# Optimization experiments

Hardware: AMD Instinct MI355X
Metric: run time of the kernel (lower is better)

Reference implementation:

```python
import math
import jax, jax.numpy as jnp
import numpy as np

MAX_LEN = 1024

def _sinusoidal_pe(seq_len, d_model):
    pos = jnp.arange(seq_len, dtype=jnp.float32)[:, None]
    div = jnp.exp(jnp.arange(0, d_model, 2, dtype=jnp.float32) * (-math.log(10000.0) / d_model))
    ang = pos * div  # [S, D/2]
    pe = jnp.zeros((seq_len, d_model), dtype=jnp.float32)
    pe = pe.at[:, 0::2].set(jnp.sin(ang))
    pe = pe.at[:, 1::2].set(jnp.cos(ang))
    return pe

def setup_inputs() -> dict:
    key = jax.random.key(0)
    ks = jax.random.split(key, 4)
    B, S, D, H = 4, 1024, 1024, 16
    x = jax.random.normal(ks[0], (B, S, D), dtype=jnp.float32)
    gamma = jnp.ones((D,), dtype=jnp.float32)
    beta = jnp.zeros((D,), dtype=jnp.float32)
    w_pos = jax.random.normal(ks[1], (2 * D, D), dtype=jnp.float32) * (1.0 / math.sqrt(D))
    w_tok = jax.random.normal(ks[2], (3 * D, D), dtype=jnp.float32) * (1.0 / math.sqrt(D))
    bias_table = jax.random.normal(ks[3], (2 * MAX_LEN, H), dtype=jnp.float32) * 0.02
    return {"x": x, "gamma": gamma, "beta": beta, "w_pos": w_pos, "w_tok": w_tok, "bias_table": bias_table}

def reference(x, gamma, beta, w_pos, w_tok, bias_table):
    B, S, D = x.shape
    H = bias_table.shape[1]
    dh = D // H
    scale = 1.0 / math.sqrt(2 * dh)

    # untied positional scores (identical across batch)
    pe = _sinusoidal_pe(S, D)                      # [S, D]
    pos = pe @ w_pos.T                             # [S, 2D]
    pos_k, pos_q = pos[:, :D], pos[:, D:]
    pos_k = pos_k.reshape(S, H, dh)
    pos_q = pos_q.reshape(S, H, dh)
    pos_attn = jnp.einsum('qhd,khd->hqk', pos_q, pos_k)  # [H, S, S]

    # token scores
    mu = jnp.mean(x, axis=-1, keepdims=True)
    var = jnp.mean((x - mu) ** 2, axis=-1, keepdims=True)
    xn = (x - mu) / jnp.sqrt(var + 1e-5) * gamma + beta
    tok = xn @ w_tok.T                             # [B, S, 3D]
    tok_k, tok_q, tok_v = jnp.split(tok, 3, axis=-1)
    tok_k = tok_k.reshape(B, S, H, dh)
    tok_q = tok_q.reshape(B, S, H, dh)
    tok_v = tok_v.reshape(B, S, H, dh)
    tok_attn = jnp.einsum('bqhd,bkhd->bhqk', tok_q, tok_k)  # [B, H, S, S]

    attn = (tok_attn + pos_attn[None]) / scale

    # relative-position bias
    rel = jnp.arange(S)[None, :] - jnp.arange(S)[:, None] + MAX_LEN  # [S, S]
    bias = bias_table[rel]                         # [S, S, H]
    attn = attn + jnp.transpose(bias, (2, 0, 1))[None]

    attn = jax.nn.softmax(attn, axis=-1)
    out = jnp.einsum('bhqk,bkhd->bqhd', attn, tok_v)
    return out.reshape(B, S, D)
```

## Files before the change

### kernel.cpp

```cpp
#include <hip/hip_runtime.h>
#include <math.h>

#define SB 1024
#define DM 1024
#define BB 4
#define NH 16
#define DH 64
#define ML 1024

typedef __attribute__((ext_vector_type(8))) short short8;
typedef __attribute__((ext_vector_type(8))) _Float16 half8;
typedef __attribute__((ext_vector_type(4))) float f32x4;
typedef unsigned short u16;

__device__ __forceinline__ u16 f2bf(float x) {
  unsigned u = __float_as_uint(x);
  u += 0x7fffu + ((u >> 16) & 1u);
  return (u16)(u >> 16);
}
__device__ __forceinline__ float bf2f(u16 h) { return __uint_as_float((unsigned)h << 16); }

__device__ __forceinline__ void async16(void* lds, const void* g) {
  __builtin_amdgcn_global_load_lds(
      (const __attribute__((address_space(1))) unsigned*)g,
      (__attribute__((address_space(3))) unsigned*)lds, 16, 0, 0);
}


__device__ __forceinline__ void pack16_body(int rt, int t, const float* __restrict__ src,
    _Float16* __restrict__ dH, _Float16* __restrict__ dL, float scale) {
  int r16 = t >> 4, ks = t & 15;
  const float* sp = src + (size_t)(rt * 16 + r16) * 1024 + ks * 64;
  float v[64];
  #pragma unroll
  for (int i = 0; i < 16; ++i) {
    float4 f = *(const float4*)(sp + i * 4);
    v[i*4+0] = f.x; v[i*4+1] = f.y; v[i*4+2] = f.z; v[i*4+3] = f.w;
  }
  #pragma unroll
  for (int hf = 0; hf < 2; ++hf) {
    int kt = ks * 2 + hf;
    #pragma unroll
    for (int gg = 0; gg < 4; ++gg) {
      half8 hv, lv;
      #pragma unroll
      for (int j = 0; j < 8; ++j) {
        float x = v[hf * 32 + gg * 8 + j] * scale;
        _Float16 h = (_Float16)x;
        hv[j] = h;
        lv[j] = (_Float16)(x - (float)h);
      }
      size_t off = ((size_t)(rt * 32 + kt) * 64 + r16 + gg * 16) * 8;
      *(half8*)(dH + off) = hv;
      *(half8*)(dL + off) = lv;
    }
  }
}

__device__ __forceinline__ void pe_pack_body(int rt, int t,
    _Float16* __restrict__ dH, _Float16* __restrict__ dL) {
  int r16 = t >> 4, ks = t & 15;
  int p = rt * 16 + r16;
  float v[64];
  #pragma unroll
  for (int i = 0; i < 32; ++i) {
    int c0 = ks * 64 + 2 * i;
    float div = exp2f((float)c0 * (-0.01297628162065376f));
    float ang = (float)p * div;
    v[2*i]   = __sinf(ang);
    v[2*i+1] = __cosf(ang);
  }
  #pragma unroll
  for (int hf = 0; hf < 2; ++hf) {
    int kt = ks * 2 + hf;
    #pragma unroll
    for (int gg = 0; gg < 4; ++gg) {
      half8 hv, lv;
      #pragma unroll
      for (int j = 0; j < 8; ++j) {
        float x = v[hf * 32 + gg * 8 + j];
        _Float16 h = (_Float16)x;
        hv[j] = h;
        lv[j] = (_Float16)(x - (float)h);
      }
      size_t off = ((size_t)(rt * 32 + kt) * 64 + r16 + gg * 16) * 8;
      *(half8*)(dH + off) = hv;
      *(half8*)(dL + off) = lv;
    }
  }
}

__device__ __forceinline__ void ln_pack_body(int rt, int t, const float* __restrict__ x,
    const float* __restrict__ gamma, const float* __restrict__ beta,
    _Float16* __restrict__ dH, _Float16* __restrict__ dL) {
  int r16 = t >> 4, ks = t & 15;
  const float* sp = x + (size_t)(rt * 16 + r16) * 1024 + ks * 64;
  float v[64];
  float s1 = 0.f, s2 = 0.f;
  #pragma unroll
  for (int i = 0; i < 16; ++i) {
    float4 f = *(const float4*)(sp + i * 4);
    v[i*4+0] = f.x; v[i*4+1] = f.y; v[i*4+2] = f.z; v[i*4+3] = f.w;
    s1 += f.x + f.y + f.z + f.w;
    s2 += f.x*f.x + f.y*f.y + f.z*f.z + f.w*f.w;
  }
  #pragma unroll
  for (int off = 1; off < 16; off <<= 1) {
    s1 += __shfl_xor(s1, off, 64);
    s2 += __shfl_xor(s2, off, 64);
  }
  float mu = s1 * (1.0f / 1024.0f);
  float var = s2 * (1.0f / 1024.0f) - mu * mu;
  float rstd = rsqrtf(var + 1e-5f);
  #pragma unroll
  for (int hf = 0; hf < 2; ++hf) {
    int kt = ks * 2 + hf;
    #pragma unroll
    for (int gg = 0; gg < 4; ++gg) {
      const float* gp = gamma + ks * 64 + hf * 32 + gg * 8;
      const float* bp = beta  + ks * 64 + hf * 32 + gg * 8;
      half8 hv, lv;
      #pragma unroll
      for (int j = 0; j < 8; ++j) {
        float xn = (v[hf * 32 + gg * 8 + j] - mu) * rstd * gp[j] + bp[j];
        _Float16 h = (_Float16)xn;
        hv[j] = h;
        lv[j] = (_Float16)(xn - (float)h);
      }
      size_t off = ((size_t)(rt * 32 + kt) * 64 + r16 + gg * 16) * 8;
      *(half8*)(dH + off) = hv;
      *(half8*)(dL + off) = lv;
    }
  }
}

__global__ __launch_bounds__(256) void prep_all(
    const float* __restrict__ x, const float* __restrict__ gamma,
    const float* __restrict__ beta,
    const float* __restrict__ w_pos, const float* __restrict__ w_tok,
    _Float16* __restrict__ peH, _Float16* __restrict__ peL,
    _Float16* __restrict__ xnH, _Float16* __restrict__ xnL,
    _Float16* __restrict__ wpH, _Float16* __restrict__ wpL,
    _Float16* __restrict__ wtH, _Float16* __restrict__ wtL) {
  int bid = blockIdx.x;
  int t = threadIdx.x;
  if (bid < 64)       pe_pack_body(bid, t, peH, peL);
  else if (bid < 320) ln_pack_body(bid - 64, t, x, gamma, beta, xnH, xnL);
  else if (bid < 448) pack16_body(bid - 320, t, w_pos, wpH, wpL, 32.0f);
  else                pack16_body(bid - 448, t, w_tok, wtH, wtL, 32.0f);
}

__global__ __launch_bounds__(256, 2) void gemm16p(
    const _Float16* __restrict__ AtH, const _Float16* __restrict__ AtL,
    const _Float16* __restrict__ ApH, const _Float16* __restrict__ ApL,
    const _Float16* __restrict__ BtH, const _Float16* __restrict__ BtL,
    const _Float16* __restrict__ BpH, const _Float16* __restrict__ BpL,
    u16* __restrict__ KtfH, u16* __restrict__ KtfL,
    u16* __restrict__ KpfH, u16* __restrict__ KpfL,
    u16* __restrict__ QH, u16* __restrict__ QL,
    u16* __restrict__ pQH, u16* __restrict__ pQL,
    u16* __restrict__ vF, float sK, float sQ, float sV) {
  __shared__ _Float16 L[32 * 512];
  int t = threadIdx.x;
  int wv = t >> 6, lane = t & 63;
  int wm = wv >> 1, wn = wv & 1;
  int r16 = lane & 15, g = lane >> 4;

  int phys = blockIdx.x;
  int bid = (phys & 7) * 56 + (phys >> 3);
  bool isPos = (bid >= 384);
  int idx = isPos ? bid - 384 : bid;
  int n0, m0;
  const _Float16 *AH, *AL, *BH, *BL;
  if (isPos) { n0 = (idx & 7) * 256;  m0 = (idx >> 3) * 128;
               AH = ApH; AL = ApL; BH = BpH; BL = BpL; }
  else       { n0 = (idx % 12) * 256; m0 = (idx / 12) * 128;
               AH = AtH; AL = AtL; BH = BtH; BL = BtL; }
  int mt0 = m0 >> 4, nt0 = n0 >> 4;
  bool split = isPos || (n0 < 2048);

  f32x4 acc[4][8];
  #pragma unroll
  for (int i = 0; i < 4; ++i)
    #pragma unroll
    for (int j = 0; j < 8; ++j) acc[i][j] = (f32x4){0.f, 0.f, 0.f, 0.f};

  for (int kt = 0; kt < 32; ++kt) {
    __syncthreads();
    #pragma unroll
    for (int rd = 0; rd < 8; ++rd) {
      int ci = rd * 4 + wv;
      bool isAlo = (ci < 16) && (ci & 1);
      if (!split && isAlo) continue;
      const _Float16* src;
      if (ci < 16) {
        int mt = ci >> 1, pl = ci & 1;
        const _Float16* P = pl ? AL : AH;
        src = P + ((size_t)((mt0 + mt) * 32 + kt) * 64 + lane) * 8;
      } else {
        int nt = ci - 16;
        src = BH + ((size_t)((nt0 + nt) * 32 + kt) * 64 + lane) * 8;
      }
      async16(&L[ci * 512], src);
    }
    half8 blo[8];
    if (split) {
      #pragma unroll
      for (int j = 0; j < 8; ++j) {
        int ntg = nt0 + wn * 8 + j;
        blo[j] = *(const half8*)(BL + ((size_t)(ntg * 32 + kt) * 64 + lane) * 8);
      }
    }
    __syncthreads();

    half8 ah[4], al[4];
    #pragma unroll
    for (int i = 0; i < 4; ++i)
      ah[i] = *(const half8*)&L[(((wm * 4 + i) * 2 + 0) * 512) + lane * 8];
    if (split) {
      #pragma unroll
      for (int i = 0; i < 4; ++i)
        al[i] = *(const half8*)&L[(((wm * 4 + i) * 2 + 1) * 512) + lane * 8];
    }
    #pragma unroll
    for (int j = 0; j < 8; ++j) {
      half8 bh = *(const half8*)&L[((16 + wn * 8 + j) * 512) + lane * 8];
      #pragma unroll
      for (int i = 0; i < 4; ++i) {
        acc[i][j] = __builtin_amdgcn_mfma_f32_16x16x32_f16(ah[i], bh, acc[i][j], 0, 0, 0);
        if (split) {
          acc[i][j] = __builtin_amdgcn_mfma_f32_16x16x32_f16(al[i], bh, acc[i][j], 0, 0, 0);
          acc[i][j] = __builtin_amdgcn_mfma_f32_16x16x32_f16(ah[i], blo[j], acc[i][j], 0, 0, 0);
        }
      }
    }
  }

  int band = n0 >> 10;
  u16* fKH = isPos ? KpfH : KtfH;
  u16* fKL = isPos ? KpfL : KtfL;
  u16* qHo = isPos ? pQH  : QH;
  u16* qLo = isPos ? pQL  : QL;
  if (band == 1) {
    #pragma unroll
    for (int i = 0; i < 4; ++i)
      #pragma unroll
      for (int j = 0; j < 8; ++j) {
        int lc = (n0 & 1023) + wn * 128 + j * 16 + r16;
        #pragma unroll
        for (int reg = 0; reg < 4; ++reg) {
          int row = m0 + wm * 64 + i * 16 + g * 4 + reg;
          float cv = acc[i][j][reg] * sQ;
          u16 hi = f2bf(cv);
          qHo[(size_t)row * 1024 + lc] = hi;
          qLo[(size_t)row * 1024 + lc] = f2bf(cv - bf2f(hi));
        }
      }
  } else if (band == 0) {
    #pragma unroll
    for (int i = 0; i < 4; ++i)
      #pragma unroll
      for (int j = 0; j < 8; ++j) {
        int colg = n0 + wn * 128 + j * 16 + r16;
        int h = colg >> 6, dc = colg & 63;
        #pragma unroll
        for (int reg = 0; reg < 4; ++reg) {
          int row = m0 + wm * 64 + i * 16 + g * 4 + reg;
          int bhK = (row >> 10) * NH + h;
          size_t a = ((size_t)((bhK * 64 + ((row & 1023) >> 4)) * 2 + (dc >> 5)) << 9)
                   + ((row & 15) + 16 * ((dc >> 3) & 3)) * 8 + (dc & 7);
          float cv = acc[i][j][reg] * sK;
          u16 hi = f2bf(cv);
          fKH[a] = hi;
          fKL[a] = f2bf(cv - bf2f(hi));
        }
      }
  } else {
    #pragma unroll
    for (int i = 0; i < 4; ++i)
      #pragma unroll
      for (int j = 0; j < 8; ++j) {
        int colg = (n0 & 1023) + wn * 128 + j * 16 + r16;
        int h = colg >> 6, dc = colg & 63;
        #pragma unroll
        for (int reg = 0; reg < 4; ++reg) {
          int row = m0 + wm * 64 + i * 16 + g * 4 + reg;
          int s = row & 1023;
          size_t a = ((size_t)((((row >> 10) * NH + h) * 32 + (s >> 5)) * 4 + (dc >> 4)) << 9)
                   + ((s >> 3) & 3) * 128 + (s & 7) + (dc & 15) * 8;
          vF[a] = f2bf(acc[i][j][reg] * sV);
        }
      }
  }
}

__global__ __launch_bounds__(256, 2) void gemm16m(
    const _Float16* __restrict__ AtH, const _Float16* __restrict__ AtL,
    const _Float16* __restrict__ ApH, const _Float16* __restrict__ ApL,
    const float* __restrict__ Wt, const float* __restrict__ Wp,
    u16* __restrict__ KtfH, u16* __restrict__ KtfL,
    u16* __restrict__ KpfH, u16* __restrict__ KpfL,
    u16* __restrict__ QH, u16* __restrict__ QL,
    u16* __restrict__ pQH, u16* __restrict__ pQL,
    u16* __restrict__ vF, float sK, float sQ, float sV) {
  __shared__ _Float16 L[48 * 512];
  int t = threadIdx.x;
  int wv = t >> 6, lane = t & 63;
  int wm = wv >> 1, wn = wv & 1;
  int r16 = lane & 15, g = lane >> 4;

  int phys = blockIdx.x;
  int bid = (phys & 7) * 56 + (phys >> 3);
  bool isPos = (bid >= 384);
  int idx = isPos ? bid - 384 : bid;
  int n0, m0;
  const _Float16 *AH, *AL;
  const float* W;
  if (isPos) { n0 = (idx & 7) * 256;  m0 = (idx >> 3) * 128; AH = ApH; AL = ApL; W = Wp; }
  else       { n0 = (idx % 12) * 256; m0 = (idx / 12) * 128; AH = AtH; AL = AtL; W = Wt; }
  int mt0 = m0 >> 4, nt0 = n0 >> 4;
  bool split = isPos || (n0 < 2048);

  f32x4 acc[4][8];
  #pragma unroll
  for (int i = 0; i < 4; ++i)
    #pragma unroll
    for (int j = 0; j < 8; ++j) acc[i][j] = (f32x4){0.f, 0.f, 0.f, 0.f};

  for (int kt = 0; kt < 32; ++kt) {
    __syncthreads();
    #pragma unroll
    for (int rd = 0; rd < 4; ++rd) {
      int ci = rd * 4 + wv;
      int mt = ci >> 1, pl = ci & 1;
      if (!split && pl) continue;
      const _Float16* src = (pl ? AL : AH)
          + ((size_t)((mt0 + mt) * 32 + kt) * 64 + lane) * 8;
      async16(&L[ci * 512], src);
    }
    #pragma unroll
    for (int tt = 0; tt < 4; ++tt) {
      int nt = wv * 4 + tt;
      const float* wsrc = W + (size_t)((nt0 + nt) * 16 + r16) * 1024 + kt * 32 + g * 8;
      float4 w0 = *(const float4*)wsrc;
      float4 w1 = *(const float4*)(wsrc + 4);
      float wvv[8] = {w0.x, w0.y, w0.z, w0.w, w1.x, w1.y, w1.z, w1.w};
      half8 hv, lv;
      #pragma unroll
      for (int j = 0; j < 8; ++j) {
        float xx = wvv[j] * 32.0f;
        _Float16 h = (_Float16)xx;
        hv[j] = h;
        lv[j] = (_Float16)(xx - (float)h);
      }
      *(half8*)&L[(16 + nt) * 512 + lane * 8] = hv;
      if (split) *(half8*)&L[(32 + nt) * 512 + lane * 8] = lv;
    }
    __syncthreads();

    half8 ah[4], al[4];
    #pragma unroll
    for (int i = 0; i < 4; ++i)
      ah[i] = *(const half8*)&L[(((wm * 4 + i) * 2 + 0) * 512) + lane * 8];
    if (split) {
      #pragma unroll
      for (int i = 0; i < 4; ++i)
        al[i] = *(const half8*)&L[(((wm * 4 + i) * 2 + 1) * 512) + lane * 8];
    }
    #pragma unroll
    for (int j = 0; j < 8; ++j) {
      half8 bh = *(const half8*)&L[((16 + wn * 8 + j) * 512) + lane * 8];
      #pragma unroll
      for (int i = 0; i < 4; ++i) {
        acc[i][j] = __builtin_amdgcn_mfma_f32_16x16x32_f16(ah[i], bh, acc[i][j], 0, 0, 0);
        if (split) {
          half8 bl = *(const half8*)&L[((32 + wn * 8 + j) * 512) + lane * 8];
          acc[i][j] = __builtin_amdgcn_mfma_f32_16x16x32_f16(al[i], bh, acc[i][j], 0, 0, 0);
          acc[i][j] = __builtin_amdgcn_mfma_f32_16x16x32_f16(ah[i], bl, acc[i][j], 0, 0, 0);
        }
      }
    }
  }

  int band = n0 >> 10;
  u16* fKH = isPos ? KpfH : KtfH;
  u16* fKL = isPos ? KpfL : KtfL;
  u16* qHo = isPos ? pQH  : QH;
  u16* qLo = isPos ? pQL  : QL;
  if (band == 1) {
    #pragma unroll
    for (int i = 0; i < 4; ++i)
      #pragma unroll
      for (int j = 0; j < 8; ++j) {
        int lc = (n0 & 1023) + wn * 128 + j * 16 + r16;
        #pragma unroll
        for (int reg = 0; reg < 4; ++reg) {
          int row = m0 + wm * 64 + i * 16 + g * 4 + reg;
          float cv = acc[i][j][reg] * sQ;
          u16 hi = f2bf(cv);
          qHo[(size_t)row * 1024 + lc] = hi;
          qLo[(size_t)row * 1024 + lc] = f2bf(cv - bf2f(hi));
        }
      }
  } else if (band == 0) {
    #pragma unroll
    for (int i = 0; i < 4; ++i)
      #pragma unroll
      for (int j = 0; j < 8; ++j) {
        int colg = n0 + wn * 128 + j * 16 + r16;
        int h = colg >> 6, dc = colg & 63;
        #pragma unroll
        for (int reg = 0; reg < 4; ++reg) {
          int row = m0 + wm * 64 + i * 16 + g * 4 + reg;
          int bhK = (row >> 10) * NH + h;
          size_t a = ((size_t)((bhK * 64 + ((row & 1023) >> 4)) * 2 + (dc >> 5)) << 9)
                   + ((row & 15) + 16 * ((dc >> 3) & 3)) * 8 + (dc & 7);
          float cv = acc[i][j][reg] * sK;
          u16 hi = f2bf(cv);
          fKH[a] = hi;
          fKL[a] = f2bf(cv - bf2f(hi));
        }
      }
  } else {
    #pragma unroll
    for (int i = 0; i < 4; ++i)
      #pragma unroll
      for (int j = 0; j < 8; ++j) {
        int colg = (n0 & 1023) + wn * 128 + j * 16 + r16;
        int h = colg >> 6, dc = colg & 63;
        #pragma unroll
        for (int reg = 0; reg < 4; ++reg) {
          int row = m0 + wm * 64 + i * 16 + g * 4 + reg;
          int s = row & 1023;
          size_t a = ((size_t)((((row >> 10) * NH + h) * 32 + (s >> 5)) * 4 + (dc >> 4)) << 9)
                   + ((s >> 3) & 3) * 128 + (s & 7) + (dc & 15) * 8;
          vF[a] = f2bf(acc[i][j][reg] * sV);
        }
      }
  }
}

__global__ __launch_bounds__(256, 2) void attn_mfma10(
    const u16* __restrict__ KtfH, const u16* __restrict__ KtfL,
    const u16* __restrict__ KpfH, const u16* __restrict__ KpfL,
    const u16* __restrict__ QHg, const u16* __restrict__ QLg,
    const u16* __restrict__ pQH, const u16* __restrict__ pQL,
    const u16* __restrict__ Vf,
    const float* __restrict__ bt,
    float* __restrict__ out) {
  __shared__ u16 Klds[5 * 4096];
  __shared__ float biasL[2 * ML];
  __shared__ u16 Pb[4][16 * 72];

  int phys = blockIdx.x;
  int bid = (phys & 7) * 64 + (phys >> 3);
  int qt = bid & 7;
  int bh = bid >> 3;
  int b = bh >> 4, h = bh & 15;
  int q0 = qt * 128;
  int t = threadIdx.x;
  int wv = t >> 6, lane = t & 63;
  int g = lane >> 4, r16 = lane & 15;
  int lo = lane * 8;

  #pragma unroll
  for (int k = 0; k < 8; ++k)
    biasL[t + k * 256] = bt[(size_t)(t + k * 256) * NH + h];

  short8 qhi[2][4], qlo[2][4];
  #pragma unroll
  for (int cc = 0; cc < 2; ++cc) {
    int qrow = q0 + wv * 32 + cc * 16 + r16;
    #pragma unroll
    for (int c = 0; c < 4; ++c) {
      if (c < 2) {
        size_t off = (size_t)(b * SB + qrow) * 1024 + h * DH + c * 32 + g * 8;
        qhi[cc][c] = *(const short8*)(QHg + off);
        qlo[cc][c] = *(const short8*)(QLg + off);
      } else {
        size_t off = (size_t)qrow * 1024 + h * DH + (c - 2) * 32 + g * 8;
        qhi[cc][c] = *(const short8*)(pQH + off);
        qlo[cc][c] = *(const short8*)(pQL + off);
      }
    }
  }

  f32x4 O[2][4];
  #pragma unroll
  for (int cc = 0; cc < 2; ++cc)
    #pragma unroll
    for (int dt = 0; dt < 4; ++dt) O[cc][dt] = (f32x4){0.f, 0.f, 0.f, 0.f};
  float m_run[2][4], l_run[2][4];
  #pragma unroll
  for (int cc = 0; cc < 2; ++cc)
    #pragma unroll
    for (int reg = 0; reg < 4; ++reg) { m_run[cc][reg] = -3e38f; l_run[cc][reg] = 0.f; }

  int qb0 = q0 + wv * 32 + g * 4;
  const u16* ktHb = KtfH + (size_t)(bh * 64) * 1024;
  const u16* ktLb = KtfL + (size_t)(bh * 64) * 1024;
  const u16* kpHb = KpfH + (size_t)(h * 64) * 1024;
  const u16* kpLb = KpfL + (size_t)(h * 64) * 1024;
  const u16* vb   = Vf   + (size_t)(bh * 32) * 2048;
  int bb = ML + r16 - qb0;

  for (int ktr = 0; ktr < 16; ++ktr) {
    __syncthreads();

    {
      int p0 = wv * 512, p1 = (wv + 4) * 512;
      async16(&Klds[0 * 4096 + p0], ktHb + p0 + lo);
      async16(&Klds[0 * 4096 + p1], ktHb + p1 + lo);
      async16(&Klds[1 * 4096 + p0], ktLb + p0 + lo);
      async16(&Klds[1 * 4096 + p1], ktLb + p1 + lo);
      async16(&Klds[2 * 4096 + p0], kpHb + p0 + lo);
      async16(&Klds[2 * 4096 + p1], kpHb + p1 + lo);
      async16(&Klds[3 * 4096 + p0], kpLb + p0 + lo);
      async16(&Klds[3 * 4096 + p1], kpLb + p1 + lo);
      async16(&Klds[4 * 4096 + p0], vb + p0 + lo);
      async16(&Klds[4 * 4096 + p1], vb + p1 + lo);
    }

    float bias[2][4][4];
    #pragma unroll
    for (int nt = 0; nt < 4; ++nt)
      #pragma unroll
      for (int reg = 0; reg < 4; ++reg) {
        bias[0][nt][reg] = biasL[bb + nt * 16 - reg];
        bias[1][nt][reg] = biasL[bb - 16 + nt * 16 - reg];
      }

    asm volatile("s_waitcnt vmcnt(0)" ::: "memory");
    __syncthreads();

    f32x4 S[2][4];
    #pragma unroll
    for (int nt = 0; nt < 4; ++nt) {
      f32x4 a0 = (f32x4){0.f, 0.f, 0.f, 0.f};
      f32x4 a1 = (f32x4){0.f, 0.f, 0.f, 0.f};
      #pragma unroll
      for (int c = 0; c < 4; ++c) {
        int ch = (c < 2) ? 0 : 2;
        int co = c & 1;
        short8 bhi = *(const short8*)&Klds[(ch + 0) * 4096 + nt * 1024 + co * 512 + lo];
        short8 blo = *(const short8*)&Klds[(ch + 1) * 4096 + nt * 1024 + co * 512 + lo];
        a0 = __builtin_amdgcn_mfma_f32_16x16x32_bf16(qhi[0][c], bhi, a0, 0, 0, 0);
        a1 = __builtin_amdgcn_mfma_f32_16x16x32_bf16(qhi[1][c], bhi, a1, 0, 0, 0);
        a0 = __builtin_amdgcn_mfma_f32_16x16x32_bf16(qlo[0][c], bhi, a0, 0, 0, 0);
        a1 = __builtin_amdgcn_mfma_f32_16x16x32_bf16(qlo[1][c], bhi, a1, 0, 0, 0);
        a0 = __builtin_amdgcn_mfma_f32_16x16x32_bf16(qhi[0][c], blo, a0, 0, 0, 0);
        a1 = __builtin_amdgcn_mfma_f32_16x16x32_bf16(qhi[1][c], blo, a1, 0, 0, 0);
      }
      S[0][nt] = a0; S[1][nt] = a1;
    }

    short8 vfrag[2][4];
    #pragma unroll
    for (int kc = 0; kc < 2; ++kc)
      #pragma unroll
      for (int dt = 0; dt < 4; ++dt)
        vfrag[kc][dt] = *(const short8*)&Klds[4 * 4096 + (kc * 4 + dt) * 512 + lo];

    #pragma unroll
    for (int cc = 0; cc < 2; ++cc)
      #pragma unroll
      for (int nt = 0; nt < 4; ++nt)
        #pragma unroll
        for (int reg = 0; reg < 4; ++reg)
          S[cc][nt][reg] += bias[cc][nt][reg];

    float tm[2][4], al[2][4];
    #pragma unroll
    for (int cc = 0; cc < 2; ++cc)
      #pragma unroll
      for (int reg = 0; reg < 4; ++reg)
        tm[cc][reg] = fmaxf(fmaxf(S[cc][0][reg], S[cc][1][reg]),
                            fmaxf(S[cc][2][reg], S[cc][3][reg]));
    #pragma unroll
    for (int off = 1; off < 16; off <<= 1)
      #pragma unroll
      for (int cc = 0; cc < 2; ++cc)
        #pragma unroll
        for (int reg = 0; reg < 4; ++reg)
          tm[cc][reg] = fmaxf(tm[cc][reg], __shfl_xor(tm[cc][reg], off, 64));
    #pragma unroll
    for (int cc = 0; cc < 2; ++cc)
      #pragma unroll
      for (int reg = 0; reg < 4; ++reg) {
        float mn = fmaxf(m_run[cc][reg], tm[cc][reg]);
        al[cc][reg] = __expf(m_run[cc][reg] - mn);
        m_run[cc][reg] = mn;
      }
    float ts[2][4] = {{0.f, 0.f, 0.f, 0.f}, {0.f, 0.f, 0.f, 0.f}};
    #pragma unroll
    for (int cc = 0; cc < 2; ++cc)
      #pragma unroll
      for (int nt = 0; nt < 4; ++nt)
        #pragma unroll
        for (int reg = 0; reg < 4; ++reg) {
          float p = __expf(S[cc][nt][reg] - m_run[cc][reg]);
          S[cc][nt][reg] = p;
          ts[cc][reg] += p;
        }
    #pragma unroll
    for (int cc = 0; cc < 2; ++cc)
      #pragma unroll
      for (int reg = 0; reg < 4; ++reg)
        l_run[cc][reg] = l_run[cc][reg] * al[cc][reg] + ts[cc][reg];
    #pragma unroll
    for (int cc = 0; cc < 2; ++cc)
      #pragma unroll
      for (int dt = 0; dt < 4; ++dt)
        #pragma unroll
        for (int reg = 0; reg < 4; ++reg)
          O[cc][dt][reg] *= al[cc][reg];

    #pragma unroll
    for (int cc = 0; cc < 2; ++cc) {
      u16* pb = Pb[wv];
      #pragma unroll
      for (int nt = 0; nt < 4; ++nt)
        #pragma unroll
        for (int reg = 0; reg < 4; ++reg)
          pb[(g * 4 + reg) * 72 + nt * 16 + r16] = f2bf(S[cc][nt][reg]);
      #pragma unroll
      for (int kc = 0; kc < 2; ++kc) {
        short8 pa = *(const short8*)&Pb[wv][r16 * 72 + kc * 32 + g * 8];
        #pragma unroll
        for (int dt = 0; dt < 4; ++dt)
          O[cc][dt] = __builtin_amdgcn_mfma_f32_16x16x32_bf16(pa, vfrag[kc][dt], O[cc][dt], 0, 0, 0);
      }
    }

    ktHb += 4096; ktLb += 4096; kpHb += 4096; kpLb += 4096;
    vb += 4096; bb += 64;
  }

  #pragma unroll
  for (int off = 1; off < 16; off <<= 1)
    #pragma unroll
    for (int cc = 0; cc < 2; ++cc)
      #pragma unroll
      for (int reg = 0; reg < 4; ++reg)
        l_run[cc][reg] += __shfl_xor(l_run[cc][reg], off, 64);
  #pragma unroll
  for (int cc = 0; cc < 2; ++cc)
    #pragma unroll
    for (int reg = 0; reg < 4; ++reg) l_run[cc][reg] = 1.0f / l_run[cc][reg];
  #pragma unroll
  for (int cc = 0; cc < 2; ++cc)
    #pragma unroll
    for (int dt = 0; dt < 4; ++dt)
      #pragma unroll
      for (int reg = 0; reg < 4; ++reg)
        out[(size_t)(b * SB + qb0 + cc * 16 + reg) * DM + h * DH + dt * 16 + r16] =
            O[cc][dt][reg] * l_run[cc][reg];
}

extern "C" void kernel_launch(void* const* d_in, const int* in_sizes, int n_in,
                              void* d_out, int out_size, void* d_ws, size_t ws_size,
                              hipStream_t stream) {
  const float* x     = (const float*)d_in[0];
  const float* gamma = (const float*)d_in[1];
  const float* beta  = (const float*)d_in[2];
  const float* w_pos = (const float*)d_in[3];
  const float* w_tok = (const float*)d_in[4];
  const float* bt    = (const float*)d_in[5];
  float* out = (float*)d_out;
  float* ws  = (float*)d_ws;
  const size_t M1 = 1u << 20;
  const float IS = 11.313708498984761f;

  u16 *KtfH, *KtfL, *KpfH, *KpfL, *QH, *QL, *posQH, *posQL, *Vf;

  if (ws_size >= 22 * M1 * 4) {
    _Float16* peH = (_Float16*)(ws);
    _Float16* peL = (_Float16*)(ws + M1 / 2);
    _Float16* xnH = (_Float16*)(ws + 1 * M1);
    _Float16* xnL = (_Float16*)(ws + 3 * M1);
    _Float16* wpH = (_Float16*)(ws + 5 * M1);
    _Float16* wpL = (_Float16*)(ws + 6 * M1);
    _Float16* wtH = (_Float16*)(ws + 7 * M1);
    _Float16* wtL = (_Float16*)(ws + 8 * M1 + M1/2);
    KpfH  = (u16*)(ws + 10 * M1);
    KpfL  = (u16*)(ws + 10 * M1 + M1 / 2);
    posQH = (u16*)(ws + 11 * M1);
    posQL = (u16*)(ws + 11 * M1 + M1 / 2);
    KtfH  = (u16*)(ws + 12 * M1);
    KtfL  = (u16*)(ws + 14 * M1);
    QH    = (u16*)(ws + 16 * M1);
    QL    = (u16*)(ws + 18 * M1);
    Vf    = (u16*)(ws + 20 * M1);

    prep_all<<<640, 256, 0, stream>>>(x, gamma, beta, w_pos, w_tok,
        peH, peL, xnH, xnL, wpH, wpL, wtH, wtL);
    gemm16p<<<448, 256, 0, stream>>>(
        xnH, xnL, peH, peL, wtH, wtL, wpH, wpL,
        KtfH, KtfL, KpfH, KpfL, QH, QL, posQH, posQL, Vf,
        1.0f / 32.0f, IS / 32.0f, 1.0f / 32.0f);
  } else {
    _Float16* peH = (_Float16*)(ws);
    _Float16* peL = (_Float16*)(ws + M1 / 2);
    _Float16* xnH = (_Float16*)(ws + 1 * M1);
    _Float16* xnL = (_Float16*)(ws + 3 * M1);
    KpfH  = (u16*)(ws + 5 * M1);
    KpfL  = (u16*)(ws + 5 * M1 + M1 / 2);
    posQH = (u16*)(ws + 6 * M1);
    posQL = (u16*)(ws + 6 * M1 + M1 / 2);
    KtfH  = (u16*)(ws + 7 * M1);
    KtfL  = (u16*)(ws + 9 * M1);
    QH    = (u16*)(ws + 11 * M1);
    QL    = (u16*)(ws + 13 * M1);
    Vf    = (u16*)(ws + 15 * M1);

    prep_all<<<320, 256, 0, stream>>>(x, gamma, beta, w_pos, w_tok,
        peH, peL, xnH, xnL, (_Float16*)nullptr, (_Float16*)nullptr,
        (_Float16*)nullptr, (_Float16*)nullptr);
    gemm16m<<<448, 256, 0, stream>>>(
        xnH, xnL, peH, peL, w_tok, w_pos,
        KtfH, KtfL, KpfH, KpfL, QH, QL, posQH, posQL, Vf,
        1.0f / 32.0f, IS / 32.0f, 1.0f / 32.0f);
  }

  attn_mfma10<<<BB * NH * (SB / 128), 256, 0, stream>>>(
      KtfH, KtfL, KpfH, KpfL, QH, QL, posQH, posQL, Vf, bt, out);
}
```

Measured before the change: 253.6 us.

## Stage prep rows through LDS for coalesced loads and finer-grained blocks

Rewrites the prep/pack kernel so each block loads 8 full rows with coalesced float4 reads into a padded LDS tile, then repacks into the split-fp16 MFMA layout from LDS. Previously each thread read 64 contiguous floats of a row, giving strided, poorly coalesced global loads. LayerNorm statistics are now reduced through shuffles plus a small LDS array. The grid doubles to 8-row tiles with a higher occupancy bound, at the cost of extra syncthreads and LDS traffic. Only the prep stage changes, a small part of total time.

```diff
diff --git a/kernel.cpp b/kernel.cpp
--- a/kernel.cpp
+++ b/kernel.cpp
@@ -26,115 +26,9 @@
       (__attribute__((address_space(3))) unsigned*)lds, 16, 0, 0);
 }
 
-
-__device__ __forceinline__ void pack16_body(int rt, int t, const float* __restrict__ src,
-    _Float16* __restrict__ dH, _Float16* __restrict__ dL, float scale) {
-  int r16 = t >> 4, ks = t & 15;
-  const float* sp = src + (size_t)(rt * 16 + r16) * 1024 + ks * 64;
-  float v[64];
-  #pragma unroll
-  for (int i = 0; i < 16; ++i) {
-    float4 f = *(const float4*)(sp + i * 4);
-    v[i*4+0] = f.x; v[i*4+1] = f.y; v[i*4+2] = f.z; v[i*4+3] = f.w;
-  }
-  #pragma unroll
-  for (int hf = 0; hf < 2; ++hf) {
-    int kt = ks * 2 + hf;
-    #pragma unroll
-    for (int gg = 0; gg < 4; ++gg) {
-      half8 hv, lv;
-      #pragma unroll
-      for (int j = 0; j < 8; ++j) {
-        float x = v[hf * 32 + gg * 8 + j] * scale;
-        _Float16 h = (_Float16)x;
-        hv[j] = h;
-        lv[j] = (_Float16)(x - (float)h);
-      }
-      size_t off = ((size_t)(rt * 32 + kt) * 64 + r16 + gg * 16) * 8;
-      *(half8*)(dH + off) = hv;
-      *(half8*)(dL + off) = lv;
-    }
-  }
-}
-
-__device__ __forceinline__ void pe_pack_body(int rt, int t,
-    _Float16* __restrict__ dH, _Float16* __restrict__ dL) {
-  int r16 = t >> 4, ks = t & 15;
-  int p = rt * 16 + r16;
-  float v[64];
-  #pragma unroll
-  for (int i = 0; i < 32; ++i) {
-    int c0 = ks * 64 + 2 * i;
-    float div = exp2f((float)c0 * (-0.01297628162065376f));
-    float ang = (float)p * div;
-    v[2*i]   = __sinf(ang);
-    v[2*i+1] = __cosf(ang);
-  }
-  #pragma unroll
-  for (int hf = 0; hf < 2; ++hf) {
-    int kt = ks * 2 + hf;
-    #pragma unroll
-    for (int gg = 0; gg < 4; ++gg) {
-      half8 hv, lv;
-      #pragma unroll
-      for (int j = 0; j < 8; ++j) {
-        float x = v[hf * 32 + gg * 8 + j];
-        _Float16 h = (_Float16)x;
-        hv[j] = h;
-        lv[j] = (_Float16)(x - (float)h);
-      }
-      size_t off = ((size_t)(rt * 32 + kt) * 64 + r16 + gg * 16) * 8;
-      *(half8*)(dH + off) = hv;
-      *(half8*)(dL + off) = lv;
-    }
-  }
-}
-
-__device__ __forceinline__ void ln_pack_body(int rt, int t, const float* __restrict__ x,
-    const float* __restrict__ gamma, const float* __restrict__ beta,
-    _Float16* __restrict__ dH, _Float16* __restrict__ dL) {
-  int r16 = t >> 4, ks = t & 15;
-  const float* sp = x + (size_t)(rt * 16 + r16) * 1024 + ks * 64;
-  float v[64];
-  float s1 = 0.f, s2 = 0.f;
-  #pragma unroll
-  for (int i = 0; i < 16; ++i) {
-    float4 f = *(const float4*)(sp + i * 4);
-    v[i*4+0] = f.x; v[i*4+1] = f.y; v[i*4+2] = f.z; v[i*4+3] = f.w;
-    s1 += f.x + f.y + f.z + f.w;
-    s2 += f.x*f.x + f.y*f.y + f.z*f.z + f.w*f.w;
-  }
-  #pragma unroll
-  for (int off = 1; off < 16; off <<= 1) {
-    s1 += __shfl_xor(s1, off, 64);
-    s2 += __shfl_xor(s2, off, 64);
-  }
-  float mu = s1 * (1.0f / 1024.0f);
-  float var = s2 * (1.0f / 1024.0f) - mu * mu;
-  float rstd = rsqrtf(var + 1e-5f);
-  #pragma unroll
-  for (int hf = 0; hf < 2; ++hf) {
-    int kt = ks * 2 + hf;
-    #pragma unroll
-    for (int gg = 0; gg < 4; ++gg) {
-      const float* gp = gamma + ks * 64 + hf * 32 + gg * 8;
-      const float* bp = beta  + ks * 64 + hf * 32 + gg * 8;
-      half8 hv, lv;
-      #pragma unroll
-      for (int j = 0; j < 8; ++j) {
-        float xn = (v[hf * 32 + gg * 8 + j] - mu) * rstd * gp[j] + bp[j];
-        _Float16 h = (_Float16)xn;
-        hv[j] = h;
-        lv[j] = (_Float16)(xn - (float)h);
-      }
-      size_t off = ((size_t)(rt * 32 + kt) * 64 + r16 + gg * 16) * 8;
-      *(half8*)(dH + off) = hv;
-      *(half8*)(dL + off) = lv;
-    }
-  }
-}
-
-__global__ __launch_bounds__(256) void prep_all(
+#define TPITCH 1028
+
+__global__ __launch_bounds__(256, 4) void prep_all(
     const float* __restrict__ x, const float* __restrict__ gamma,
     const float* __restrict__ beta,
     const float* __restrict__ w_pos, const float* __restrict__ w_tok,
@@ -142,12 +36,103 @@
     _Float16* __restrict__ xnH, _Float16* __restrict__ xnL,
     _Float16* __restrict__ wpH, _Float16* __restrict__ wpL,
     _Float16* __restrict__ wtH, _Float16* __restrict__ wtL) {
-  int bid = blockIdx.x;
-  int t = threadIdx.x;
-  if (bid < 64)       pe_pack_body(bid, t, peH, peL);
-  else if (bid < 320) ln_pack_body(bid - 64, t, x, gamma, beta, xnH, xnL);
-  else if (bid < 448) pack16_body(bid - 320, t, w_pos, wpH, wpL, 32.0f);
-  else                pack16_body(bid - 448, t, w_tok, wtH, wtL, 32.0f);
+  __shared__ float T[8 * TPITCH];
+  __shared__ float Sred[4][8][2];
+
+  int bid = blockIdx.x, t = threadIdx.x;
+  int wv = t >> 6, lane = t & 63;
+
+  int type, rt;
+  const float* src = nullptr;
+  _Float16 *dH, *dL;
+  if (bid < 128)      { type = 0; rt = bid;       dH = peH; dL = peL; }
+  else if (bid < 640) { type = 1; rt = bid - 128; src = x;     dH = xnH; dL = xnL; }
+  else if (bid < 896) { type = 2; rt = bid - 640; src = w_pos; dH = wpH; dL = wpL; }
+  else                { type = 2; rt = bid - 896; src = w_tok; dH = wtH; dL = wtL; }
+
+  if (type == 0) {
+    float div0 = exp2f((float)(t * 4)     * (-0.01297628162065376f));
+    float div1 = exp2f((float)(t * 4 + 2) * (-0.01297628162065376f));
+    #pragma unroll
+    for (int i = 0; i < 8; ++i) {
+      float p = (float)(rt * 8 + i);
+      float a0 = p * div0, a1 = p * div1;
+      float4 f;
+      f.x = __sinf(a0); f.y = __cosf(a0);
+      f.z = __sinf(a1); f.w = __cosf(a1);
+      *(float4*)&T[i * TPITCH + t * 4] = f;
+    }
+  } else if (type == 1) {
+    #pragma unroll
+    for (int i = 0; i < 8; ++i) {
+      float4 f = *(const float4*)(src + (size_t)(rt * 8 + i) * 1024 + t * 4);
+      *(float4*)&T[i * TPITCH + t * 4] = f;
+    }
+  } else {
+    #pragma unroll
+    for (int i = 0; i < 8; ++i) {
+      float4 f = *(const float4*)(src + (size_t)(rt * 8 + i) * 1024 + t * 4);
+      f.x *= 32.f; f.y *= 32.f; f.z *= 32.f; f.w *= 32.f;
+      *(float4*)&T[i * TPITCH + t * 4] = f;
+    }
+  }
+  __syncthreads();
+
+  if (type == 1) {
+    int row = t & 7, cc = t >> 3;
+    float s1 = 0.f, s2 = 0.f;
+    #pragma unroll
+    for (int i = 0; i < 8; ++i) {
+      float4 f = *(const float4*)&T[row * TPITCH + cc * 32 + i * 4];
+      s1 += f.x + f.y + f.z + f.w;
+      s2 += f.x*f.x + f.y*f.y + f.z*f.z + f.w*f.w;
+    }
+    s1 += __shfl_xor(s1, 8, 64);  s2 += __shfl_xor(s2, 8, 64);
+    s1 += __shfl_xor(s1, 16, 64); s2 += __shfl_xor(s2, 16, 64);
+    s1 += __shfl_xor(s1, 32, 64); s2 += __shfl_xor(s2, 32, 64);
+    if (lane < 8) { Sred[wv][lane][0] = s1; Sred[wv][lane][1] = s2; }
+  }
+  __syncthreads();
+
+  int row = lane & 7, gg = (lane >> 3) & 3, ktp = lane >> 5;
+  float mu = 0.f, rs = 0.f;
+  if (type == 1) {
+    float s1 = Sred[0][row][0] + Sred[1][row][0] + Sred[2][row][0] + Sred[3][row][0];
+    float s2 = Sred[0][row][1] + Sred[1][row][1] + Sred[2][row][1] + Sred[3][row][1];
+    mu = s1 * (1.0f / 1024.0f);
+    float var = s2 * (1.0f / 1024.0f) - mu * mu;
+    rs = rsqrtf(var + 1e-5f);
+  }
+  int grow16 = rt >> 1;
+  int rsub = (rt & 1) * 8 + row;
+  #pragma unroll
+  for (int q = 0; q < 4; ++q) {
+    int kt = wv * 8 + q * 2 + ktp;
+    int col = kt * 32 + gg * 8;
+    float v[8];
+    *(float4*)&v[0] = *(const float4*)&T[row * TPITCH + col];
+    *(float4*)&v[4] = *(const float4*)&T[row * TPITCH + col + 4];
+    if (type == 1) {
+      float4 gp0 = *(const float4*)(gamma + col);
+      float4 gp1 = *(const float4*)(gamma + col + 4);
+      float4 bp0 = *(const float4*)(beta + col);
+      float4 bp1 = *(const float4*)(beta + col + 4);
+      v[0] = (v[0]-mu)*rs*gp0.x + bp0.x;  v[1] = (v[1]-mu)*rs*gp0.y + bp0.y;
+      v[2] = (v[2]-mu)*rs*gp0.z + bp0.z;  v[3] = (v[3]-mu)*rs*gp0.w + bp0.w;
+      v[4] = (v[4]-mu)*rs*gp1.x + bp1.x;  v[5] = (v[5]-mu)*rs*gp1.y + bp1.y;
+      v[6] = (v[6]-mu)*rs*gp1.z + bp1.z;  v[7] = (v[7]-mu)*rs*gp1.w + bp1.w;
+    }
+    half8 hv, lv;
+    #pragma unroll
+    for (int j = 0; j < 8; ++j) {
+      _Float16 h = (_Float16)v[j];
+      hv[j] = h;
+      lv[j] = (_Float16)(v[j] - (float)h);
+    }
+    size_t off = ((size_t)(grow16 * 32 + kt) * 64 + rsub + gg * 16) * 8;
+    *(half8*)(dH + off) = hv;
+    *(half8*)(dL + off) = lv;
+  }
 }
 
 __global__ __launch_bounds__(256, 2) void gemm16p(
@@ -692,7 +677,7 @@
     QL    = (u16*)(ws + 18 * M1);
     Vf    = (u16*)(ws + 20 * M1);
 
-    prep_all<<<640, 256, 0, stream>>>(x, gamma, beta, w_pos, w_tok,
+    prep_all<<<1280, 256, 0, stream>>>(x, gamma, beta, w_pos, w_tok,
         peH, peL, xnH, xnL, wpH, wpL, wtH, wtL);
     gemm16p<<<448, 256, 0, stream>>>(
         xnH, xnL, peH, peL, wtH, wtL, wpH, wpL,
@@ -713,7 +698,7 @@
     QL    = (u16*)(ws + 13 * M1);
     Vf    = (u16*)(ws + 15 * M1);
 
-    prep_all<<<320, 256, 0, stream>>>(x, gamma, beta, w_pos, w_tok,
+    prep_all<<<640, 256, 0, stream>>>(x, gamma, beta, w_pos, w_tok,
         peH, peL, xnH, xnL, (_Float16*)nullptr, (_Float16*)nullptr,
         (_Float16*)nullptr, (_Float16*)nullptr);
     gemm16m<<<448, 256, 0, stream>>>(
```

Result: faster. 244.2 us (-3.7%).
